# Performance work log

Measured on AMD Instinct MI355X. Metric: run time of the kernel, lower is better.

The kernel has to match this reference:

```python
import jax, jax.numpy as jnp
import numpy as np

A = 100000          # num atoms
E = 1600000         # num edges
N_SPECIES = 4       # len(atomic_types)
N_RADIAL = 8        # l=1 radial functions (max_radial hyper)
N_PSEUDO = 4        # Alchemical pseudo species
D = N_RADIAL * N_PSEUDO  # embedding_dim = 32
RC = 5.0            # cutoff radius
WIDTH = 0.5         # shifted-cosine width


def setup_inputs() -> dict:
    key = jax.random.key(0)
    ks = jax.random.split(key, 9)
    return {
        "interatomic_vectors": jax.random.normal(ks[0], (E, 3), dtype=jnp.float32),
        "centers": jax.random.randint(ks[1], (E,), 0, A),
        "neighbors": jax.random.randint(ks[2], (E,), 0, A),
        "species": jax.random.randint(ks[3], (A,), 0, N_SPECIES),
        "structures": jnp.sort(jax.random.randint(ks[4], (A,), 0, 64)),
        "atom_index_in_structure": jax.random.randint(ks[5], (A,), 0, A),
        # learned params
        "W_alch": jax.random.normal(ks[6], (N_SPECIES, N_PSEUDO), dtype=jnp.float32) * 0.1,
        "center_embedding": jax.random.normal(ks[7], (N_SPECIES, D), dtype=jnp.float32),
        "W_contract": jax.random.normal(ks[8], (3, D), dtype=jnp.float32) * (1.0 / np.sqrt(D)),
    }


def _shifted_cosine(d):
    # 1 below rc-width, smooth cosine taper to 0 at rc
    inner = RC - WIDTH
    taper = 0.5 * (jnp.cos(jnp.pi * (d - inner) / WIDTH) + 1.0)
    return jnp.where(d < inner, 1.0, jnp.where(d < RC, taper, 0.0))


def reference(interatomic_vectors, centers, neighbors, species, structures,
              atom_index_in_structure, W_alch, center_embedding, W_contract):
    eps = 1e-12
    d = jnp.sqrt(jnp.sum(interatomic_vectors * interatomic_vectors, axis=1) + eps)  # (E,)
    fc = _shifted_cosine(d)                                                         # (E,)
    # Laplacian-eigenstate-style l=1 radial basis: sin(n*pi*d/rc)/d, n=1..N_RADIAL
    n = jnp.arange(1, N_RADIAL + 1, dtype=jnp.float32)
    R = jnp.sin(n[None, :] * (jnp.pi / RC) * d[:, None]) / d[:, None]               # (E, nR)
    # real l=1 spherical harmonics, m order (-1, 0, 1) -> (y, z, x)/d
    Y = interatomic_vectors[:, jnp.array([1, 2, 0])] / d[:, None]                   # (E, 3)
    # alchemical pseudo-species weights of the neighbor
    alch = W_alch[species[neighbors]]                                               # (E, nQ)
    # per-edge expansion coefficients, scattered onto centers
    edge = (fc[:, None, None, None]
            * Y[:, :, None, None]
            * R[:, None, :, None]
            * alch[:, None, None, :])                                               # (E, 3, nR, nQ)
    spex = jax.ops.segment_sum(edge, centers, num_segments=A)                       # (A, 3, nR, nQ)
    x = spex.reshape(A, 3, D)                                                       # reshape(n,q -> n*q)
    x = x * center_embedding[species][:, None, :]                                   # center encoding
    out = jnp.einsum("amd,od->amo", x, W_contract)                                  # (A, 3, 3)
    return out
```

## Files before the change

kernel.cpp:

```cpp
#include <hip/hip_runtime.h>
#include <hip/hip_fp16.h>


constexpr int NSP  = 4;
constexpr int NRAD = 8;
constexpr int NPS  = 4;
constexpr int DDIM = NRAD * NPS;

constexpr int APB      = 128;
constexpr int APB_SH   = 7;
constexpr int NBIN_PAD = 832;
constexpr int PH1_BLK  = 512;
constexpr int PH1_U    = 4;
constexpr int PH1_REC  = PH1_BLK * PH1_U;
constexpr int CAP2     = 2560;
constexpr int OVF_CAP  = 65536;

__device__ __forceinline__ unsigned pack2(float a, float b) {
    union { __half2 h; unsigned u; } cv;
    cv.h = __floats2half2_rn(a, b);
    return cv.u;
}
__device__ __forceinline__ float2 unpack2(unsigned u) {
    union { unsigned u; __half2 h; } cv;
    cv.u = u;
    return __half22float2(cv.h);
}

__device__ __forceinline__ void build_w2(
    float* sW2, const float* cemb, const float* Wc, const float* W_alch,
    int tid, int nthreads)
{
    for (int i = tid; i < 3 * NRAD * 16; i += nthreads) {
        int p  = i & 15;
        int n  = (i >> 4) & 7;
        int o  = i >> 7;
        int sc = p >> 2, sn = p & 3;
        float w = 0.0f;
        #pragma unroll
        for (int q = 0; q < NPS; q++)
            w += cemb[sc * DDIM + n * NPS + q] * Wc[o * DDIM + n * NPS + q]
               * W_alch[sn * NPS + q];
        sW2[i] = w;
    }
}

__device__ __forceinline__ bool edge_math(
    float vx, float vy, float vz, int pair, const float* sW2,
    float g[3], float t[3])
{
    float d2    = vx * vx + vy * vy + vz * vz + 1e-12f;
    float d     = sqrtf(d2);
    float inv_d = 1.0f / d;

    const float PI = 3.14159265358979323846f;
    const float RCUT = 5.0f, INNER = 4.5f, INVW = 2.0f;
    if (d >= RCUT) return false;
    float taper = 0.5f * (cosf(PI * (d - INNER) * INVW) + 1.0f);
    float fc = (d < INNER) ? 1.0f : taper;

    float theta = (PI / RCUT) * d;
    float s1 = sinf(theta);
    float c1 = cosf(theta);
    float two_c = 2.0f * c1;
    float R[NRAD];
    R[0] = s1 * inv_d;
    float sm2 = 0.0f, sm1 = s1;
    #pragma unroll
    for (int n = 1; n < NRAD; n++) {
        float s = two_c * sm1 - sm2;
        sm2 = sm1; sm1 = s;
        R[n] = s * inv_d;
    }

    #pragma unroll
    for (int o = 0; o < 3; o++) {
        float acc = 0.0f;
        #pragma unroll
        for (int n = 0; n < NRAD; n++)
            acc += R[n] * sW2[(o * NRAD + n) * 16 + pair];
        t[o] = acc;
    }
    g[0] = fc * vy * inv_d;
    g[1] = fc * vz * inv_d;
    g[2] = fc * vx * inv_d;
    return true;
}

__global__ __launch_bounds__(PH1_BLK) void vb_phase1(
    const float* __restrict__ vecs,
    const int*   __restrict__ centers,
    const int*   __restrict__ neighbors,
    const int*   __restrict__ species,
    const float* __restrict__ W_alch,
    const float* __restrict__ cemb,
    const float* __restrict__ Wc,
    int*         __restrict__ gcursor,
    int*         __restrict__ ovfcnt,
    int4*        __restrict__ ovf,
    int4*        __restrict__ payload,
    int E, int nbin, int cap)
{
    __shared__ float sW2[3 * NRAD * 16];
    __shared__ int4  srec[PH1_REC];
    __shared__ int lcount[NBIN_PAD], lexcl[NBIN_PAD],
                   lbase[NBIN_PAD], lcur[NBIN_PAD];
    __shared__ int sTotal;

    int tid = threadIdx.x;
    build_w2(sW2, cemb, Wc, W_alch, tid, PH1_BLK);
    for (int i = tid; i < NBIN_PAD; i += PH1_BLK) lcount[i] = 0;
    __syncthreads();

    int4 rec[PH1_U];
    #pragma unroll
    for (int u = 0; u < PH1_U; u++) {
        int e = blockIdx.x * PH1_REC + u * PH1_BLK + tid;
        rec[u].x = -1;
        if (e < E) {
            float vx = vecs[3 * e + 0];
            float vy = vecs[3 * e + 1];
            float vz = vecs[3 * e + 2];
            int c  = centers[e];
            int pair = species[c] * 4 + species[neighbors[e]];
            float g[3], t[3];
            if (edge_math(vx, vy, vz, pair, sW2, g, t)) {
                rec[u].x = c;
                rec[u].y = (int)pack2(g[0], g[1]);
                rec[u].z = (int)pack2(g[2], t[0]);
                rec[u].w = (int)pack2(t[1], t[2]);
                atomicAdd(&lcount[c >> APB_SH], 1);
            }
        }
    }
    __syncthreads();

    if (tid < 64) {
        int base = tid * 13;
        int pre[13];
        int sum = 0;
        #pragma unroll
        for (int j = 0; j < 13; j++) { pre[j] = sum; sum += lcount[base + j]; }
        int incl = sum;
        #pragma unroll
        for (int off = 1; off < 64; off <<= 1) {
            int t = __shfl_up(incl, off, 64);
            if (tid >= off) incl += t;
        }
        int ex = incl - sum;
        #pragma unroll
        for (int j = 0; j < 13; j++) lexcl[base + j] = ex + pre[j];
        if (tid == 63) sTotal = incl;
    }
    __syncthreads();

    for (int i = tid; i < nbin; i += PH1_BLK) {
        lcur[i] = lexcl[i];
        int n = lcount[i];
        lbase[i] = n ? atomicAdd(&gcursor[i], n) : 0;
    }
    __syncthreads();

    #pragma unroll
    for (int u = 0; u < PH1_U; u++) {
        if (rec[u].x >= 0) {
            int bin = rec[u].x >> APB_SH;
            int p = atomicAdd(&lcur[bin], 1);
            srec[p] = rec[u];
        }
    }
    __syncthreads();

    int total = sTotal;
    for (int i = tid; i < total; i += PH1_BLK) {
        int4 r = srec[i];
        int bin  = r.x >> APB_SH;
        int slot = lbase[bin] + (i - lexcl[bin]);
        if (slot < cap) {
            payload[(size_t)bin * cap + slot] = r;
        } else {
            int p = atomicAdd(ovfcnt, 1);
            if (p < OVF_CAP) ovf[p] = r;
        }
    }
}

__global__ __launch_bounds__(256) void vb_phase2(
    const int*  __restrict__ gcursor,
    const int*  __restrict__ ovfcnt,
    const int4* __restrict__ ovf,
    const int4* __restrict__ payload,
    float*      __restrict__ out,
    int A, int cap)
{
    __shared__ int4 srec2[CAP2];
    __shared__ unsigned short sidx[CAP2];
    __shared__ int cnt[APB], aexcl[APB], ccur[APB];
    __shared__ float sout[APB * 9];

    int b   = blockIdx.x;
    int tid = threadIdx.x;
    int count = min(gcursor[b], cap);
    const int4* pb = payload + (size_t)b * cap;

    float acc[9] = {0,0,0,0,0,0,0,0,0};
    int myatom = (b << APB_SH) + tid;

    for (int base = 0; base < count; base += CAP2) {
        int nc = min(count - base, CAP2);
        if (tid < APB) cnt[tid] = 0;
        __syncthreads();

        for (int i = tid; i < nc; i += 256) {
            int4 r = pb[base + i];
            srec2[i] = r;
            atomicAdd(&cnt[r.x & (APB - 1)], 1);
        }
        __syncthreads();

        if (tid < 64) {
            int c0 = cnt[2 * tid], c1 = cnt[2 * tid + 1];
            int s1 = c0 + c1;
            int incl = s1;
            #pragma unroll
            for (int off = 1; off < 64; off <<= 1) {
                int t = __shfl_up(incl, off, 64);
                if (tid >= off) incl += t;
            }
            int ex = incl - s1;
            aexcl[2 * tid]     = ex;
            aexcl[2 * tid + 1] = ex + c0;
        }
        __syncthreads();
        if (tid < APB) ccur[tid] = aexcl[tid];
        __syncthreads();

        for (int i = tid; i < nc; i += 256) {
            int k = srec2[i].x & (APB - 1);
            sidx[atomicAdd(&ccur[k], 1)] = (unsigned short)i;
        }
        __syncthreads();

        if (tid < APB) {
            int st = aexcl[tid], en = st + cnt[tid];
            for (int j = st; j < en; j++) {
                int4 r = srec2[sidx[j]];
                float2 g01 = unpack2((unsigned)r.y);
                float2 g2t = unpack2((unsigned)r.z);
                float2 t12 = unpack2((unsigned)r.w);
                float g0 = g01.x, g1 = g01.y, g2 = g2t.x;
                float t0 = g2t.y, t1 = t12.x, t2 = t12.y;
                acc[0] += g0 * t0; acc[1] += g0 * t1; acc[2] += g0 * t2;
                acc[3] += g1 * t0; acc[4] += g1 * t1; acc[5] += g1 * t2;
                acc[6] += g2 * t0; acc[7] += g2 * t1; acc[8] += g2 * t2;
            }
        }
        __syncthreads();
    }

    int novf = min(*ovfcnt, OVF_CAP);
    for (int i = 0; i < novf; i++) {
        int4 r = ovf[i];
        if (tid < APB && r.x == myatom) {
            float2 g01 = unpack2((unsigned)r.y);
            float2 g2t = unpack2((unsigned)r.z);
            float2 t12 = unpack2((unsigned)r.w);
            float g0 = g01.x, g1 = g01.y, g2 = g2t.x;
            float t0 = g2t.y, t1 = t12.x, t2 = t12.y;
            acc[0] += g0 * t0; acc[1] += g0 * t1; acc[2] += g0 * t2;
            acc[3] += g1 * t0; acc[4] += g1 * t1; acc[5] += g1 * t2;
            acc[6] += g2 * t0; acc[7] += g2 * t1; acc[8] += g2 * t2;
        }
    }

    if (tid < APB) {
        #pragma unroll
        for (int k = 0; k < 9; k++) sout[tid * 9 + k] = acc[k];
    }
    __syncthreads();
    size_t gbase = (size_t)b * APB * 9;
    size_t lim = (size_t)A * 9;
    for (int i = tid; i < APB * 9; i += 256) {
        size_t gi = gbase + i;
        if (gi < lim) out[gi] = sout[i];
    }
}

__global__ __launch_bounds__(256) void vb_edge_fallback(
    const float* __restrict__ vecs,
    const int*   __restrict__ centers,
    const int*   __restrict__ neighbors,
    const int*   __restrict__ species,
    const float* __restrict__ W_alch,
    const float* __restrict__ cemb,
    const float* __restrict__ Wc,
    float*       __restrict__ out,
    int E)
{
    __shared__ float sW2[3 * NRAD * 16];
    build_w2(sW2, cemb, Wc, W_alch, threadIdx.x, blockDim.x);
    __syncthreads();

    int e = blockIdx.x * blockDim.x + threadIdx.x;
    if (e >= E) return;
    float vx = vecs[3 * e + 0], vy = vecs[3 * e + 1], vz = vecs[3 * e + 2];
    int c = centers[e];
    int pair = species[c] * 4 + species[neighbors[e]];
    float g[3], t[3];
    if (!edge_math(vx, vy, vz, pair, sW2, g, t)) return;
    float* op = out + (size_t)c * 9;
    #pragma unroll
    for (int m = 0; m < 3; m++)
        #pragma unroll
        for (int o = 0; o < 3; o++)
            atomicAdd(op + m * 3 + o, g[m] * t[o]);
}

extern "C" void kernel_launch(void* const* d_in, const int* in_sizes, int n_in,
                              void* d_out, int out_size, void* d_ws, size_t ws_size,
                              hipStream_t stream) {
    const float* vecs      = (const float*)d_in[0];
    const int*   centers   = (const int*)d_in[1];
    const int*   neighbors = (const int*)d_in[2];
    const int*   species   = (const int*)d_in[3];
    const float* W_alch    = (const float*)d_in[6];
    const float* cemb      = (const float*)d_in[7];
    const float* Wc        = (const float*)d_in[8];
    float*       out       = (float*)d_out;

    int E = in_sizes[1];
    int A = in_sizes[3];
    int nbin = (A + APB - 1) >> APB_SH;

    size_t ovf_off = 4096;
    size_t pay_off = ovf_off + (size_t)OVF_CAP * 16;
    long cap = 0;
    if (ws_size > pay_off) {
        cap = (long)((ws_size - pay_off) / 16) / nbin;
        cap &= ~7L;
        if (cap > 4096) cap = 4096;
    }
    long mean = (long)E / nbin + 1;

    if (nbin <= NBIN_PAD && nbin <= 3840 / 4 && cap >= mean + mean / 8) {
        int*  gcursor = (int*)d_ws;
        int*  ovfcnt  = (int*)((char*)d_ws + 3840);
        int4* ovf     = (int4*)((char*)d_ws + ovf_off);
        int4* payload = (int4*)((char*)d_ws + pay_off);
        hipMemsetAsync(d_ws, 0, 4096, stream);

        int g1 = (E + PH1_REC - 1) / PH1_REC;
        vb_phase1<<<g1, PH1_BLK, 0, stream>>>(vecs, centers, neighbors, species,
                                              W_alch, cemb, Wc,
                                              gcursor, ovfcnt, ovf, payload,
                                              E, nbin, (int)cap);
        vb_phase2<<<nbin, 256, 0, stream>>>(gcursor, ovfcnt, ovf, payload,
                                            out, A, (int)cap);
    } else {
        hipMemsetAsync(d_out, 0, (size_t)out_size * sizeof(float), stream);
        int grid = (E + 255) / 256;
        vb_edge_fallback<<<grid, 256, 0, stream>>>(vecs, centers, neighbors, species,
                                                   W_alch, cemb, Wc, out, E);
    }
}
```

Before: 144.2 us.

## Replace prefix-scan binning with fixed-capacity slot buckets in both phases

Phase 1 now claims a per-bin slot directly with a packed 16-bit shared atomic counter and stores record indices in fixed S1-wide buckets. This drops the block-wide prefix scan, the second scatter pass and several barriers. Records past the bucket capacity go to the global overflow list. Phase 2 likewise replaces its counting-sort scan with fixed S2-slot per-atom index buckets, plus a slow linear-scan fallback when an atom exceeds capacity. The trade-off is more overflow traffic, a global atomic per overflowed record, and a serial fallback if the degree distribution is skewed.

```diff
diff --git a/kernel.cpp b/kernel.cpp
--- a/kernel.cpp
+++ b/kernel.cpp
@@ -13,7 +13,9 @@
 constexpr int PH1_BLK  = 512;
 constexpr int PH1_U    = 4;
 constexpr int PH1_REC  = PH1_BLK * PH1_U;
-constexpr int CAP2     = 2560;
+constexpr int S1       = 9;
+constexpr int CAP2     = 2304;
+constexpr int S2       = 32;
 constexpr int OVF_CAP  = 65536;
 
 __device__ __forceinline__ unsigned pack2(float a, float b) {
@@ -85,6 +87,11 @@
     g[1] = fc * vz * inv_d;
     g[2] = fc * vx * inv_d;
     return true;
+}
+
+__device__ __forceinline__ void ovf_append(int* ovfcnt, int4* ovf, int4 r) {
+    int p = atomicAdd(ovfcnt, 1);
+    if (p < OVF_CAP) ovf[p] = r;
 }
 
 __global__ __launch_bounds__(PH1_BLK) void vb_phase1(
@@ -103,20 +110,18 @@
 {
     __shared__ float sW2[3 * NRAD * 16];
     __shared__ int4  srec[PH1_REC];
-    __shared__ int lcount[NBIN_PAD], lexcl[NBIN_PAD],
-                   lbase[NBIN_PAD], lcur[NBIN_PAD];
-    __shared__ int sTotal;
+    __shared__ unsigned short sidx[NBIN_PAD * S1];
+    __shared__ unsigned lcntP[NBIN_PAD / 2];
+    __shared__ unsigned short lbase[NBIN_PAD];
 
     int tid = threadIdx.x;
     build_w2(sW2, cemb, Wc, W_alch, tid, PH1_BLK);
-    for (int i = tid; i < NBIN_PAD; i += PH1_BLK) lcount[i] = 0;
-    __syncthreads();
-
-    int4 rec[PH1_U];
+    for (int i = tid; i < NBIN_PAD / 2; i += PH1_BLK) lcntP[i] = 0;
+    __syncthreads();
+
     #pragma unroll
     for (int u = 0; u < PH1_U; u++) {
         int e = blockIdx.x * PH1_REC + u * PH1_BLK + tid;
-        rec[u].x = -1;
         if (e < E) {
             float vx = vecs[3 * e + 0];
             float vy = vecs[3 * e + 1];
@@ -125,62 +130,46 @@
             int pair = species[c] * 4 + species[neighbors[e]];
             float g[3], t[3];
             if (edge_math(vx, vy, vz, pair, sW2, g, t)) {
-                rec[u].x = c;
-                rec[u].y = (int)pack2(g[0], g[1]);
-                rec[u].z = (int)pack2(g[2], t[0]);
-                rec[u].w = (int)pack2(t[1], t[2]);
-                atomicAdd(&lcount[c >> APB_SH], 1);
+                int4 r;
+                r.x = c;
+                r.y = (int)pack2(g[0], g[1]);
+                r.z = (int)pack2(g[2], t[0]);
+                r.w = (int)pack2(t[1], t[2]);
+                int bin = c >> APB_SH;
+                int sh  = (bin & 1) << 4;
+                unsigned old = atomicAdd(&lcntP[bin >> 1], 1u << sh);
+                int slot = (old >> sh) & 0xffff;
+                if (slot < S1) {
+                    int pidx = u * PH1_BLK + tid;
+                    srec[pidx] = r;
+                    sidx[bin * S1 + slot] = (unsigned short)pidx;
+                } else {
+                    ovf_append(ovfcnt, ovf, r);
+                }
             }
         }
     }
     __syncthreads();
 
-    if (tid < 64) {
-        int base = tid * 13;
-        int pre[13];
-        int sum = 0;
-        #pragma unroll
-        for (int j = 0; j < 13; j++) { pre[j] = sum; sum += lcount[base + j]; }
-        int incl = sum;
-        #pragma unroll
-        for (int off = 1; off < 64; off <<= 1) {
-            int t = __shfl_up(incl, off, 64);
-            if (tid >= off) incl += t;
-        }
-        int ex = incl - sum;
-        #pragma unroll
-        for (int j = 0; j < 13; j++) lexcl[base + j] = ex + pre[j];
-        if (tid == 63) sTotal = incl;
-    }
-    __syncthreads();
-
-    for (int i = tid; i < nbin; i += PH1_BLK) {
-        lcur[i] = lexcl[i];
-        int n = lcount[i];
-        lbase[i] = n ? atomicAdd(&gcursor[i], n) : 0;
-    }
-    __syncthreads();
-
-    #pragma unroll
-    for (int u = 0; u < PH1_U; u++) {
-        if (rec[u].x >= 0) {
-            int bin = rec[u].x >> APB_SH;
-            int p = atomicAdd(&lcur[bin], 1);
-            srec[p] = rec[u];
-        }
-    }
-    __syncthreads();
-
-    int total = sTotal;
-    for (int i = tid; i < total; i += PH1_BLK) {
-        int4 r = srec[i];
-        int bin  = r.x >> APB_SH;
-        int slot = lbase[bin] + (i - lexcl[bin]);
-        if (slot < cap) {
-            payload[(size_t)bin * cap + slot] = r;
-        } else {
-            int p = atomicAdd(ovfcnt, 1);
-            if (p < OVF_CAP) ovf[p] = r;
+    for (int b = tid; b < nbin; b += PH1_BLK) {
+        int n = (lcntP[b >> 1] >> ((b & 1) << 4)) & 0xffff;
+        n = min(n, S1);
+        if (n) lbase[b] = (unsigned short)atomicAdd(&gcursor[b], n);
+    }
+    __syncthreads();
+
+    int slots = nbin * S1;
+    for (int i = tid; i < slots; i += PH1_BLK) {
+        unsigned bin = ((unsigned)i * 7282u) >> 16;
+        int j = i - (int)bin * S1;
+        int n = (lcntP[bin >> 1] >> ((bin & 1) << 4)) & 0xffff;
+        if (j < min(n, S1)) {
+            int4 r = srec[sidx[i]];
+            int slot = (int)lbase[bin] + j;
+            if (slot < cap)
+                payload[(size_t)bin * cap + slot] = r;
+            else
+                ovf_append(ovfcnt, ovf, r);
         }
     }
 }
@@ -194,9 +183,10 @@
     int A, int cap)
 {
     __shared__ int4 srec2[CAP2];
-    __shared__ unsigned short sidx[CAP2];
-    __shared__ int cnt[APB], aexcl[APB], ccur[APB];
+    __shared__ unsigned short sidx2[S2 * APB];
+    __shared__ int cnt2[APB];
     __shared__ float sout[APB * 9];
+    __shared__ int sflag;
 
     int b   = blockIdx.x;
     int tid = threadIdx.x;
@@ -208,51 +198,51 @@
 
     for (int base = 0; base < count; base += CAP2) {
         int nc = min(count - base, CAP2);
-        if (tid < APB) cnt[tid] = 0;
+        if (tid < APB) cnt2[tid] = 0;
+        if (tid == 0) sflag = 0;
         __syncthreads();
 
         for (int i = tid; i < nc; i += 256) {
             int4 r = pb[base + i];
             srec2[i] = r;
-            atomicAdd(&cnt[r.x & (APB - 1)], 1);
+            int k = r.x & (APB - 1);
+            int slot = atomicAdd(&cnt2[k], 1);
+            if (slot < S2) sidx2[slot * APB + k] = (unsigned short)i;
+            else sflag = 1;
         }
         __syncthreads();
 
-        if (tid < 64) {
-            int c0 = cnt[2 * tid], c1 = cnt[2 * tid + 1];
-            int s1 = c0 + c1;
-            int incl = s1;
-            #pragma unroll
-            for (int off = 1; off < 64; off <<= 1) {
-                int t = __shfl_up(incl, off, 64);
-                if (tid >= off) incl += t;
+        if (tid < APB) {
+            int n = cnt2[tid];
+            if (n <= S2) {
+                for (int j = 0; j < n; j++) {
+                    int4 r = srec2[sidx2[j * APB + tid]];
+                    float2 g01 = unpack2((unsigned)r.y);
+                    float2 g2t = unpack2((unsigned)r.z);
+                    float2 t12 = unpack2((unsigned)r.w);
+                    float g0 = g01.x, g1 = g01.y, g2 = g2t.x;
+                    float t0 = g2t.y, t1 = t12.x, t2 = t12.y;
+                    acc[0] += g0 * t0; acc[1] += g0 * t1; acc[2] += g0 * t2;
+                    acc[3] += g1 * t0; acc[4] += g1 * t1; acc[5] += g1 * t2;
+                    acc[6] += g2 * t0; acc[7] += g2 * t1; acc[8] += g2 * t2;
+                }
             }
-            int ex = incl - s1;
-            aexcl[2 * tid]     = ex;
-            aexcl[2 * tid + 1] = ex + c0;
-        }
-        __syncthreads();
-        if (tid < APB) ccur[tid] = aexcl[tid];
-        __syncthreads();
-
-        for (int i = tid; i < nc; i += 256) {
-            int k = srec2[i].x & (APB - 1);
-            sidx[atomicAdd(&ccur[k], 1)] = (unsigned short)i;
-        }
-        __syncthreads();
-
-        if (tid < APB) {
-            int st = aexcl[tid], en = st + cnt[tid];
-            for (int j = st; j < en; j++) {
-                int4 r = srec2[sidx[j]];
-                float2 g01 = unpack2((unsigned)r.y);
-                float2 g2t = unpack2((unsigned)r.z);
-                float2 t12 = unpack2((unsigned)r.w);
-                float g0 = g01.x, g1 = g01.y, g2 = g2t.x;
-                float t0 = g2t.y, t1 = t12.x, t2 = t12.y;
-                acc[0] += g0 * t0; acc[1] += g0 * t1; acc[2] += g0 * t2;
-                acc[3] += g1 * t0; acc[4] += g1 * t1; acc[5] += g1 * t2;
-                acc[6] += g2 * t0; acc[7] += g2 * t1; acc[8] += g2 * t2;
+        }
+        if (sflag) {
+            if (tid < APB && cnt2[tid] > S2) {
+                for (int j = 0; j < nc; j++) {
+                    int4 r = srec2[j];
+                    if ((r.x & (APB - 1)) == tid) {
+                        float2 g01 = unpack2((unsigned)r.y);
+                        float2 g2t = unpack2((unsigned)r.z);
+                        float2 t12 = unpack2((unsigned)r.w);
+                        float g0 = g01.x, g1 = g01.y, g2 = g2t.x;
+                        float t0 = g2t.y, t1 = t12.x, t2 = t12.y;
+                        acc[0] += g0 * t0; acc[1] += g0 * t1; acc[2] += g0 * t2;
+                        acc[3] += g1 * t0; acc[4] += g1 * t1; acc[5] += g1 * t2;
+                        acc[6] += g2 * t0; acc[7] += g2 * t1; acc[8] += g2 * t2;
+                    }
+                }
             }
         }
         __syncthreads();
```

After: 269.5 us. 1.87x slower.

## Replace global-atomic bin scatter with per-block sorted runs and offset table

Applied to the files above, without the earlier changes.

Phase 1 no longer claims slots in global bins with atomics. Each block writes its locally bin-sorted records contiguously and stores a per-block table of run offsets. Phase 2 reads each block's run for its bin, prefix-sums the run lengths, and gathers the runs into shared memory in windows. This drops the memset, the global atomic cursors and the overflow path. In exchange, phase 2 must read roughly 782 offset rows per bin and perform many small uncoalesced run copies.

```diff
diff --git a/kernel.cpp b/kernel.cpp
--- a/kernel.cpp
+++ b/kernel.cpp
@@ -7,14 +7,15 @@
 constexpr int NPS  = 4;
 constexpr int DDIM = NRAD * NPS;
 
-constexpr int APB      = 128;
-constexpr int APB_SH   = 7;
-constexpr int NBIN_PAD = 832;
-constexpr int PH1_BLK  = 512;
-constexpr int PH1_U    = 4;
-constexpr int PH1_REC  = PH1_BLK * PH1_U;
-constexpr int CAP2     = 2560;
-constexpr int OVF_CAP  = 65536;
+constexpr int APB       = 128;
+constexpr int APB_SH    = 7;
+constexpr int NBIN_PAD  = 832;
+constexpr int NROWS_PAD = 832;
+constexpr int RS        = 840;
+constexpr int PH1_BLK   = 512;
+constexpr int PH1_U     = 4;
+constexpr int PH1_REC   = PH1_BLK * PH1_U;
+constexpr int CAP2      = 2304;
 
 __device__ __forceinline__ unsigned pack2(float a, float b) {
     union { __half2 h; unsigned u; } cv;
@@ -95,17 +96,16 @@
     const float* __restrict__ W_alch,
     const float* __restrict__ cemb,
     const float* __restrict__ Wc,
-    int*         __restrict__ gcursor,
-    int*         __restrict__ ovfcnt,
-    int4*        __restrict__ ovf,
+    unsigned short* __restrict__ runoff,
     int4*        __restrict__ payload,
-    int E, int nbin, int cap)
+    int E, int nbin)
 {
     __shared__ float sW2[3 * NRAD * 16];
     __shared__ int4  srec[PH1_REC];
-    __shared__ int lcount[NBIN_PAD], lexcl[NBIN_PAD],
-                   lbase[NBIN_PAD], lcur[NBIN_PAD];
-    __shared__ int sTotal;
+    __shared__ int   lcount[NBIN_PAD];
+    __shared__ int   lexcl[NBIN_PAD];
+    __shared__ int   lcur[NBIN_PAD];
+    __shared__ int   sTotal;
 
     int tid = threadIdx.x;
     build_w2(sW2, cemb, Wc, W_alch, tid, PH1_BLK);
@@ -153,12 +153,7 @@
         if (tid == 63) sTotal = incl;
     }
     __syncthreads();
-
-    for (int i = tid; i < nbin; i += PH1_BLK) {
-        lcur[i] = lexcl[i];
-        int n = lcount[i];
-        lbase[i] = n ? atomicAdd(&gcursor[i], n) : 0;
-    }
+    for (int i = tid; i < NBIN_PAD; i += PH1_BLK) lcur[i] = lexcl[i];
     __syncthreads();
 
     #pragma unroll
@@ -172,50 +167,87 @@
     __syncthreads();
 
     int total = sTotal;
-    for (int i = tid; i < total; i += PH1_BLK) {
-        int4 r = srec[i];
-        int bin  = r.x >> APB_SH;
-        int slot = lbase[bin] + (i - lexcl[bin]);
-        if (slot < cap) {
-            payload[(size_t)bin * cap + slot] = r;
-        } else {
-            int p = atomicAdd(ovfcnt, 1);
-            if (p < OVF_CAP) ovf[p] = r;
-        }
-    }
+    size_t pbase = (size_t)blockIdx.x * PH1_REC;
+    for (int i = tid; i < total; i += PH1_BLK)
+        payload[pbase + i] = srec[i];
+    unsigned short* ro = runoff + (size_t)blockIdx.x * RS;
+    for (int b = tid; b <= nbin; b += PH1_BLK)
+        ro[b] = (unsigned short)((b < nbin) ? lexcl[b] : total);
 }
 
 __global__ __launch_bounds__(256) void vb_phase2(
-    const int*  __restrict__ gcursor,
-    const int*  __restrict__ ovfcnt,
-    const int4* __restrict__ ovf,
-    const int4* __restrict__ payload,
-    float*      __restrict__ out,
-    int A, int cap)
+    const unsigned short* __restrict__ runoff,
+    const int4*           __restrict__ payload,
+    float*                __restrict__ out,
+    int A, int nblocks)
 {
     __shared__ int4 srec2[CAP2];
     __shared__ unsigned short sidx[CAP2];
+    __shared__ unsigned short sst[NROWS_PAD];
+    __shared__ unsigned short slen[NROWS_PAD];
+    __shared__ unsigned short roff[NROWS_PAD];
     __shared__ int cnt[APB], aexcl[APB], ccur[APB];
     __shared__ float sout[APB * 9];
+    __shared__ int sTotal;
 
     int b   = blockIdx.x;
     int tid = threadIdx.x;
-    int count = min(gcursor[b], cap);
-    const int4* pb = payload + (size_t)b * cap;
-
+
+    for (int r = tid; r < NROWS_PAD; r += 256) {
+        unsigned short s0 = 0, len = 0;
+        if (r < nblocks) {
+            const unsigned short* row = runoff + (size_t)r * RS + b;
+            s0 = row[0];
+            len = (unsigned short)(row[1] - row[0]);
+        }
+        sst[r] = s0;
+        slen[r] = len;
+    }
+    __syncthreads();
+
+    if (tid < 64) {
+        int base = tid * 13;
+        int pre[13];
+        int sum = 0;
+        #pragma unroll
+        for (int j = 0; j < 13; j++) { pre[j] = sum; sum += slen[base + j]; }
+        int incl = sum;
+        #pragma unroll
+        for (int off = 1; off < 64; off <<= 1) {
+            int t = __shfl_up(incl, off, 64);
+            if (tid >= off) incl += t;
+        }
+        int ex = incl - sum;
+        #pragma unroll
+        for (int j = 0; j < 13; j++)
+            roff[base + j] = (unsigned short)(ex + pre[j]);
+        if (tid == 63) sTotal = incl;
+    }
+    __syncthreads();
+
+    int total = sTotal;
     float acc[9] = {0,0,0,0,0,0,0,0,0};
-    int myatom = (b << APB_SH) + tid;
-
-    for (int base = 0; base < count; base += CAP2) {
-        int nc = min(count - base, CAP2);
+
+    for (int w0 = 0; w0 < total; w0 += CAP2) {
+        int wend = min(w0 + CAP2, total);
+        int nc = wend - w0;
+
+        for (int r = tid; r < nblocks; r += 256) {
+            int len = slen[r];
+            int ro  = roff[r];
+            if (len && ro < wend && ro + len > w0) {
+                int j0 = max(0, w0 - ro);
+                int j1 = min(len, wend - ro);
+                const int4* src = payload + (size_t)r * PH1_REC + sst[r];
+                for (int j = j0; j < j1; j++)
+                    srec2[ro + j - w0] = src[j];
+            }
+        }
         if (tid < APB) cnt[tid] = 0;
         __syncthreads();
 
-        for (int i = tid; i < nc; i += 256) {
-            int4 r = pb[base + i];
-            srec2[i] = r;
-            atomicAdd(&cnt[r.x & (APB - 1)], 1);
-        }
+        for (int i = tid; i < nc; i += 256)
+            atomicAdd(&cnt[srec2[i].x & (APB - 1)], 1);
         __syncthreads();
 
         if (tid < 64) {
@@ -258,21 +290,6 @@
         __syncthreads();
     }
 
-    int novf = min(*ovfcnt, OVF_CAP);
-    for (int i = 0; i < novf; i++) {
-        int4 r = ovf[i];
-        if (tid < APB && r.x == myatom) {
-            float2 g01 = unpack2((unsigned)r.y);
-            float2 g2t = unpack2((unsigned)r.z);
-            float2 t12 = unpack2((unsigned)r.w);
-            float g0 = g01.x, g1 = g01.y, g2 = g2t.x;
-            float t0 = g2t.y, t1 = t12.x, t2 = t12.y;
-            acc[0] += g0 * t0; acc[1] += g0 * t1; acc[2] += g0 * t2;
-            acc[3] += g1 * t0; acc[4] += g1 * t1; acc[5] += g1 * t2;
-            acc[6] += g2 * t0; acc[7] += g2 * t1; acc[8] += g2 * t2;
-        }
-    }
-
     if (tid < APB) {
         #pragma unroll
         for (int k = 0; k < 9; k++) sout[tid * 9 + k] = acc[k];
@@ -330,36 +347,26 @@
 
     int E = in_sizes[1];
     int A = in_sizes[3];
-    int nbin = (A + APB - 1) >> APB_SH;
-
-    size_t ovf_off = 4096;
-    size_t pay_off = ovf_off + (size_t)OVF_CAP * 16;
-    long cap = 0;
-    if (ws_size > pay_off) {
-        cap = (long)((ws_size - pay_off) / 16) / nbin;
-        cap &= ~7L;
-        if (cap > 4096) cap = 4096;
-    }
-    long mean = (long)E / nbin + 1;
-
-    if (nbin <= NBIN_PAD && nbin <= 3840 / 4 && cap >= mean + mean / 8) {
-        int*  gcursor = (int*)d_ws;
-        int*  ovfcnt  = (int*)((char*)d_ws + 3840);
-        int4* ovf     = (int4*)((char*)d_ws + ovf_off);
-        int4* payload = (int4*)((char*)d_ws + pay_off);
-        hipMemsetAsync(d_ws, 0, 4096, stream);
-
-        int g1 = (E + PH1_REC - 1) / PH1_REC;
-        vb_phase1<<<g1, PH1_BLK, 0, stream>>>(vecs, centers, neighbors, species,
-                                              W_alch, cemb, Wc,
-                                              gcursor, ovfcnt, ovf, payload,
-                                              E, nbin, (int)cap);
-        vb_phase2<<<nbin, 256, 0, stream>>>(gcursor, ovfcnt, ovf, payload,
-                                            out, A, (int)cap);
+    int nbin    = (A + APB - 1) >> APB_SH;
+    int nblocks = (E + PH1_REC - 1) / PH1_REC;
+
+    size_t ro_bytes = ((size_t)nblocks * RS * 2 + 255) & ~(size_t)255;
+    size_t need = ro_bytes + (size_t)nblocks * PH1_REC * 16;
+
+    if (nbin + 1 <= RS && nbin <= NBIN_PAD && nblocks <= NROWS_PAD &&
+        need <= ws_size) {
+        unsigned short* runoff = (unsigned short*)d_ws;
+        int4* payload = (int4*)((char*)d_ws + ro_bytes);
+
+        vb_phase1<<<nblocks, PH1_BLK, 0, stream>>>(vecs, centers, neighbors,
+                                                   species, W_alch, cemb, Wc,
+                                                   runoff, payload, E, nbin);
+        vb_phase2<<<nbin, 256, 0, stream>>>(runoff, payload, out, A, nblocks);
     } else {
         hipMemsetAsync(d_out, 0, (size_t)out_size * sizeof(float), stream);
         int grid = (E + 255) / 256;
-        vb_edge_fallback<<<grid, 256, 0, stream>>>(vecs, centers, neighbors, species,
-                                                   W_alch, cemb, Wc, out, E);
-    }
-}
+        vb_edge_fallback<<<grid, 256, 0, stream>>>(vecs, centers, neighbors,
+                                                   species, W_alch, cemb, Wc,
+                                                   out, E);
+    }
+}
```

Measured after the change: 147.1 us. 2.0% more time.
